# Performance work log

Measured on AMD Instinct MI355X. Metric: run time of the kernel, lower is better.

The kernel has to match this reference:

```python
import jax, jax.numpy as jnp
import numpy as np
from jax import lax

# pywt 'db6' rec_lo (scaling filter). dec_lo = rec_lo[::-1]; pytorch_wavelets
# stores dec filters flipped for conv (=correlation), so analysis correlation
# filters are exactly rec_lo and rec_hi = qmf(rec_lo). Synthesis filters for
# conv_transpose are rec_lo/rec_hi unflipped -> same arrays.
_DB6 = np.array([0.11154074335008017, 0.4946238903983854, 0.7511339080215775,
                 0.3152503517092432, -0.22626469396516913, -0.12976686756709563,
                 0.09750160558707936, 0.02752286553001629, -0.031582039318031156,
                 0.0005538422009938016, 0.004777257511010651, -0.00107730108499558],
                dtype=np.float32)
_QMF = (_DB6[::-1].copy() * ((-1.0) ** np.arange(12))).astype(np.float32)
H0, H1 = jnp.asarray(_DB6), jnp.asarray(_QMF)
LF, J = 12, 3
BATCH, SEQ_LEN, CH = 128, 720, 321
COMP_L = [99, 365, 188, 99]   # [yl, yh1, yh2, yh3] for seq_len=720
OUT_L = [22, 57, 34, 22]      # same decomposition of red_len=104


def afb1d(x):
    """One-level analysis filter bank, mode='symmetric'. x: [B,C,N]."""
    B, C, N = x.shape
    out = (N + LF - 1) // 2                      # pywt dwt_coeff_len (symmetric)
    p = 2 * (out - 1) - N + LF
    xp = jnp.pad(x, ((0, 0), (0, 0), (p // 2, (p + 1) // 2)), mode='symmetric')
    w = jnp.stack([H0, H1])[:, None, :]          # [2,1,LF]
    y = lax.conv_general_dilated(xp.reshape(B * C, 1, -1), w, (2,), 'VALID',
                                 dimension_numbers=('NCH', 'OIH', 'NCH'))
    y = y.reshape(B, C, 2, out)
    return y[:, :, 0], y[:, :, 1]


def sfb1d(lo, hi):
    """One-level synthesis bank == conv_transpose1d(stride=2, padding=LF-2)."""
    B, C, Lin = lo.shape
    z = jnp.stack([lo, hi], axis=2).reshape(B * C, 2, Lin)
    w = jnp.stack([H0[::-1], H1[::-1]])[None]    # [1,2,LF], flipped for corr
    y = lax.conv_general_dilated(z, w, (1,), ((1, 1),), lhs_dilation=(2,),
                                 dimension_numbers=('NCH', 'OIH', 'NCH'))
    return y.reshape(B, C, -1)                   # length 2*Lin + 2 - LF


def sinusoidal_pe(n_pos, d):
    pos = jnp.arange(n_pos, dtype=jnp.float32)[:, None]
    div = jnp.exp(jnp.arange(0, d, 2, dtype=jnp.float32) * (-np.log(10000.0) / d))
    pe = jnp.zeros((n_pos, d), jnp.float32)
    pe = pe.at[:, 0::2].set(jnp.sin(pos * div))
    pe = pe.at[:, 1::2].set(jnp.cos(pos * div[: d // 2]))
    return pe


def _forward(x, qws, qbs, kws, kbs, pws, pbs, iws, als, bes):
    mean = lax.stop_gradient(jnp.mean(x, axis=1, keepdims=True))
    std = lax.stop_gradient(jnp.sqrt(jnp.var(x, axis=1, keepdims=True) + 1e-5))
    xc = jnp.transpose((x - mean) / std, (0, 2, 1))      # [B,C,L]
    yl, yh = xc, []
    for _ in range(J):
        yl, hi = afb1d(yl)
        yh.append(hi)
    decomps = [yl] + yh                                  # lengths COMP_L
    preds = []
    for i, comp in enumerate(decomps):
        B, C, L = comp.shape
        Q = jnp.tanh(comp @ qws[i].T + qbs[i])           # [B,C,L]
        K = jnp.tanh(comp @ kws[i].T + kbs[i])
        scores = jnp.einsum('bcl,bcs->bls', Q, K) / (L ** 0.5)
        weighted = jnp.mean(jnp.tanh(scores), axis=1)    # [B,S] (equal per channel)
        cum = jnp.flip(jnp.cumsum(jnp.flip(weighted, -1), -1), -1)
        P = jax.nn.softmax(cum * als[i][0], axis=-1)
        idxs = jnp.arange(L, dtype=jnp.float32)
        win = jnp.sum(P * idxs, axis=-1)[:, None, None]  # soft truncation [B,1,1]
        mask = jax.nn.sigmoid((idxs[None, None, :] - win) * bes[i][0])
        pred = (comp * mask) @ pws[i].T + pbs[i]         # [B,C,O]
        pred = jax.nn.softmax(iws[i], axis=1) * (pred + sinusoidal_pe(C, pred.shape[-1])[None])
        preds.append(pred)
    ll = preds[0]
    for h in preds[:0:-1]:                               # coarsest high band first
        if ll.shape[-1] > h.shape[-1]:
            ll = ll[..., : h.shape[-1]]
        ll = sfb1d(ll, h)
    return ll, mean, std


def setup_inputs() -> dict:
    key = jax.random.key(0)
    ks = jax.random.split(key, 64)
    inp = {'x': jax.random.normal(ks[0], (BATCH, SEQ_LEN, CH), jnp.float32)}
    k = 1
    for i, (L, O) in enumerate(zip(COMP_L, OUT_L)):
        s = 1.0 / np.sqrt(L)                             # torch Linear default init
        inp[f'qw{i}'] = jax.random.uniform(ks[k], (L, L), jnp.float32, -s, s); k += 1
        inp[f'qb{i}'] = jax.random.uniform(ks[k], (L,), jnp.float32, -s, s); k += 1
        inp[f'kw{i}'] = jax.random.uniform(ks[k], (L, L), jnp.float32, -s, s); k += 1
        inp[f'kb{i}'] = jax.random.uniform(ks[k], (L,), jnp.float32, -s, s); k += 1
        inp[f'pw{i}'] = jnp.full((O, L), 1.0 / L, jnp.float32)
        inp[f'pb{i}'] = jnp.zeros((O,), jnp.float32)
        inp[f'iw{i}'] = jnp.ones((1, CH, O), jnp.float32)
        inp[f'al{i}'] = jnp.full((1,), 10.0, jnp.float32)
        inp[f'be{i}'] = jnp.full((1,), 10.0, jnp.float32)
    return inp


def reference(x, qw0, qb0, kw0, kb0, pw0, pb0, iw0, al0, be0,
              qw1, qb1, kw1, kb1, pw1, pb1, iw1, al1, be1,
              qw2, qb2, kw2, kb2, pw2, pb2, iw2, al2, be2,
              qw3, qb3, kw3, kb3, pw3, pb3, iw3, al3, be3):
    return _forward(x, [qw0, qw1, qw2, qw3], [qb0, qb1, qb2, qb3],
                    [kw0, kw1, kw2, kw3], [kb0, kb1, kb2, kb3],
                    [pw0, pw1, pw2, pw3], [pb0, pb1, pb2, pb3],
                    [iw0, iw1, iw2, iw3], [al0, al1, al2, al3],
                    [be0, be1, be2, be3])
```

## Files before the change

### kernel.cpp

```cpp
#include <hip/hip_runtime.h>
#include <hip/hip_bf16.h>
#include <math.h>

namespace {
constexpr int kB  = 128;
constexpr int kC  = 321;
constexpr int kN0 = 720;
constexpr int kCp = 384;
}

typedef __attribute__((ext_vector_type(8))) short short8;
typedef __attribute__((ext_vector_type(4))) float floatx4;

__constant__ float c_h0[12] = {
  0.11154074335008017f, 0.4946238903983854f, 0.7511339080215775f,
  0.3152503517092432f, -0.22626469396516913f, -0.12976686756709563f,
  0.09750160558707936f, 0.02752286553001629f, -0.031582039318031156f,
  0.0005538422009938016f, 0.004777257511010651f, -0.00107730108499558f};
__constant__ float c_h1[12] = {
  -0.00107730108499558f, -0.004777257511010651f, 0.0005538422009938016f,
  0.031582039318031156f, 0.02752286553001629f, -0.09750160558707936f,
  -0.12976686756709563f, 0.22626469396516913f, 0.3152503517092432f,
  -0.7511339080215775f, 0.4946238903983854f, -0.11154074335008017f};
__constant__ float c_h0r[12] = {
  -0.00107730108499558f, 0.004777257511010651f, 0.0005538422009938016f,
  -0.031582039318031156f, 0.02752286553001629f, 0.09750160558707936f,
  -0.12976686756709563f, -0.22626469396516913f, 0.3152503517092432f,
  0.7511339080215775f, 0.4946238903983854f, 0.11154074335008017f};
__constant__ float c_h1r[12] = {
  -0.11154074335008017f, 0.4946238903983854f, -0.7511339080215775f,
  0.3152503517092432f, 0.22626469396516913f, -0.12976686756709563f,
  -0.09750160558707936f, 0.02752286553001629f, 0.031582039318031156f,
  0.0005538422009938016f, -0.004777257511010651f, -0.00107730108499558f};

__device__ __forceinline__ float fast_tanh(float x) {
  float e = __expf(2.f * x);
  return 1.f - 2.f / (e + 1.f);
}
__device__ __forceinline__ unsigned short f2b(float f) {
  __hip_bfloat16 h = __float2bfloat16(f);
  return __builtin_bit_cast(unsigned short, h);
}

__device__ __forceinline__ void gload16(const unsigned short* g, short* l) {
  __builtin_amdgcn_global_load_lds(
      (const __attribute__((address_space(1))) unsigned int*)g,
      (__attribute__((address_space(3))) unsigned int*)l, 16, 0, 0);
}

__global__ void __launch_bounds__(128) partial_ms_kernel(
    const float* __restrict__ x, float* __restrict__ ps, float* __restrict__ ps2) {
  int b = blockIdx.x, chunk = blockIdx.y;
  int c = blockIdx.z * 128 + threadIdx.x;
  if (c >= kC) return;
  const float* xb = x + (size_t)b * kN0 * kC + c;
  int t0 = chunk * 90;
  float s = 0.f, s2 = 0.f;
#pragma unroll 15
  for (int i = 0; i < 90; ++i) {
    float v = xb[(size_t)(t0 + i) * kC];
    s += v; s2 += v * v;
  }
  ps [(b * 8 + chunk) * kC + c] = s;
  ps2[(b * 8 + chunk) * kC + c] = s2;
}

__global__ void __launch_bounds__(256) finalize_ms_kernel(
    const float* __restrict__ ps, const float* __restrict__ ps2,
    float* __restrict__ mout, float* __restrict__ sout,
    float* __restrict__ meanw, float* __restrict__ invw) {
  int i = blockIdx.x * 256 + threadIdx.x;
  if (i >= kB * kC) return;
  int b = i / kC, c = i - b * kC;
  float s = 0.f, s2 = 0.f;
#pragma unroll
  for (int k = 0; k < 8; ++k) { s += ps[(b * 8 + k) * kC + c]; s2 += ps2[(b * 8 + k) * kC + c]; }
  float mean = s * (1.f / (float)kN0);
  float var = s2 * (1.f / (float)kN0) - mean * mean;
  float sd = sqrtf(var + 1e-5f);
  mout[i] = mean; sout[i] = sd;
  meanw[i] = mean; invw[i] = 1.f / sd;
}

__device__ __forceinline__ int sym_reflect(int t, int N) {
  t = (t < 0) ? (-1 - t) : t;
  t = (t >= N) ? (2 * N - 1 - t) : t;
  return t;
}

template <bool NORM, bool LO_F32, bool LO_BF16>
__global__ void __launch_bounds__(256) dwt_fused_kernel(
    const float* __restrict__ in, const float* __restrict__ meanw,
    const float* __restrict__ invw, float* __restrict__ loF,
    unsigned short* __restrict__ loB, unsigned short* __restrict__ hiB,
    int N, int L, int Lp) {
  __shared__ float xs[138][64];
  __shared__ unsigned short los[64][72];
  __shared__ unsigned short his[64][72];
  const int b = blockIdx.z;
  const int n0 = blockIdx.x * 64, c0 = blockIdx.y * 64;
  const int tid = threadIdx.x;
  const int cl = tid & 63, wv = tid >> 6;
  const int c = c0 + cl;
  const int t0 = 2 * n0 - 10;
  const float* ib = in + (size_t)b * N * kC;
  float mean = 0.f, inv = 1.f;
  if (NORM && c < kC) { mean = meanw[b * kC + c]; inv = invw[b * kC + c]; }
  for (int r = wv; r < 138; r += 4) {
    int t = sym_reflect(t0 + r, N);
    float v = (c < kC) ? ib[(size_t)t * kC + c] : 0.f;
    if (NORM) v = (v - mean) * inv;
    xs[r][cl] = v;
  }
  __syncthreads();
#pragma unroll 4
  for (int k = 0; k < 16; ++k) {
    int nl = wv + 4 * k;
    int n = n0 + nl;
    float a0 = 0.f, a1 = 0.f;
    int base = 2 * nl;
#pragma unroll
    for (int j = 0; j < 12; ++j) {
      float v = xs[base + j][cl];
      a0 += v * c_h0[j]; a1 += v * c_h1[j];
    }
    bool valid = (n < L) && (c < kC);
    if (LO_F32 && valid) loF[((size_t)b * L + n) * kC + c] = a0;
    if (LO_BF16) los[cl][nl] = f2b(valid ? a0 : 0.f);
    his[cl][nl] = f2b(valid ? a1 : 0.f);
  }
  __syncthreads();
  int row = tid >> 2, part = tid & 3;
  size_t dst = ((size_t)b * kCp + c0 + row) * Lp + n0 + part * 16;
  *(uint4*)(hiB + dst)     = *(const uint4*)&his[row][part * 16];
  *(uint4*)(hiB + dst + 8) = *(const uint4*)&his[row][part * 16 + 8];
  if (LO_BF16) {
    *(uint4*)(loB + dst)     = *(const uint4*)&los[row][part * 16];
    *(uint4*)(loB + dst + 8) = *(const uint4*)&los[row][part * 16 + 8];
  }
}

struct WcArgs { const float* src[8]; unsigned short* dst[8]; int L[8]; int Lp[8]; };
__global__ void __launch_bounds__(256) wconv_all_kernel(WcArgs a) {
  int lvl = blockIdx.y;
  int Lp = a.Lp[lvl], L = a.L[lvl];
  int i = blockIdx.x * 256 + threadIdx.x;
  if (i >= Lp * Lp) return;
  int p = i / Lp, l = i - p * Lp;
  a.dst[lvl][i] = f2b((p < L && l < L) ? a.src[lvl][(size_t)p * L + l] : 0.f);
}

struct QKAllArgs {
  const unsigned short* W[8];
  const unsigned short* Xt[4];
  const float* bias[8];
  unsigned short* Y[8];
  int Lp[4], L[4], yOff[4];
};
__global__ void __launch_bounds__(512, 8) qk_all_kernel(QKAllArgs a) {
  const int y = blockIdx.y;
  const int lvl = (y >= a.yOff[1]) + (y >= a.yOff[2]) + (y >= a.yOff[3]);
  const int Lp = a.Lp[lvl], L = a.L[lvl];
  const int pBase = (y - a.yOff[lvl]) * 128;
  const unsigned short* W0 = a.W[2 * lvl]     + (size_t)pBase * Lp;
  const unsigned short* W1 = a.W[2 * lvl + 1] + (size_t)pBase * Lp;
  const int b = blockIdx.z;
  const int cBase = blockIdx.x * 64;
  const int tid = threadIdx.x;
  const int ln = tid & 63, w = tid >> 6;
  __shared__ short smem[2 * 320 * 32];
  floatx4 acc[2][4] = {};
  const unsigned short* Xb = a.Xt[lvl] + ((size_t)b * kCp + cBase) * Lp;
  const int lr = ln >> 2;
  const int ck = (ln & 3) * 8;
  const int nld = (w < 4) ? 3 : 2;
  const int ow0 = (w < 4) ? w * 3 : 12 + (w - 4) * 2;
  const unsigned short* srcs[3];
#pragma unroll
  for (int i = 0; i < 3; ++i) {
    int o = (i < nld) ? (ow0 + i) : ow0;
    int rr = o * 16 + lr;
    const unsigned short* s = (o < 8)  ? (W0 + (size_t)rr * Lp)
                            : (o < 16) ? (W1 + (size_t)(rr - 128) * Lp)
                                       : (Xb + (size_t)(rr - 256) * Lp);
    srcs[i] = s + ck;
  }
  const int nt = Lp >> 5;
#pragma unroll
  for (int i = 0; i < 3; ++i)
    if (i < nld) gload16(srcs[i], &smem[(ow0 + i) * 512]);
  __syncthreads();
  for (int kt = 0; kt < nt; ++kt) {
    if (kt + 1 < nt) {
      const int phn = ((kt + 1) & 1) * 10240;
      const int lc = (kt + 1) << 5;
#pragma unroll
      for (int i = 0; i < 3; ++i)
        if (i < nld) gload16(srcs[i] + lc, &smem[phn + (ow0 + i) * 512]);
    }
    const int ph = (kt & 1) * 10240;
    const int ko = (ln >> 4) * 8;
    const int ar = (w * 16 + (ln & 15)) * 32 + ko;
    short8 aq = *(const short8*)&smem[ph + ar];
    short8 ak = *(const short8*)&smem[ph + 4096 + ar];
    short8 bv[4];
#pragma unroll
    for (int ni = 0; ni < 4; ++ni)
      bv[ni] = *(const short8*)&smem[ph + 8192 + (ni * 16 + (ln & 15)) * 32 + ko];
#pragma unroll
    for (int ni = 0; ni < 4; ++ni) {
      acc[0][ni] = __builtin_amdgcn_mfma_f32_16x16x32_bf16(aq, bv[ni], acc[0][ni], 0, 0, 0);
      acc[1][ni] = __builtin_amdgcn_mfma_f32_16x16x32_bf16(ak, bv[ni], acc[1][ni], 0, 0, 0);
    }
    __syncthreads();
  }
#pragma unroll
  for (int s = 0; s < 2; ++s) {
    const float* bias = a.bias[2 * lvl + s];
    unsigned short* Yd = a.Y[2 * lvl + s];
#pragma unroll
    for (int r = 0; r < 4; ++r) {
      int p = pBase + w * 16 + (ln >> 4) * 4 + r;
      bool pv = (p < L);
      float bvf = pv ? bias[p] : 0.f;
#pragma unroll
      for (int ni = 0; ni < 4; ++ni) {
        int c = cBase + ni * 16 + (ln & 15);
        float v = fast_tanh(acc[s][ni][r] + bvf);
        if (s == 0) { if (!pv) v = 0.f; }
        else        { if (c >= kC) v = 0.f; }
        Yd[((size_t)b * Lp + p) * kCp + c] = f2b(v);
      }
    }
  }
}

struct ScAllArgs {
  const unsigned short* Q[4]; const unsigned short* K[4];
  float* wgt[4];
  int Lp[4], L[4], tOff[4];
  float scale[4];
};
__global__ void __launch_bounds__(512, 8) scores_all_kernel(ScAllArgs a) {
  const int t = blockIdx.x;
  const int lvl = (t >= a.tOff[1]) + (t >= a.tOff[2]) + (t >= a.tOff[3]);
  const int rel = t - a.tOff[lvl];
  const int Lp = a.Lp[lvl], L = a.L[lvl];
  const int pt = Lp >> 7;
  const int sBase = (rel % pt) * 128;
  const int lBase = (rel / pt) * 128;
  const int b = blockIdx.y;
  const int tid = threadIdx.x;
  const int ln = tid & 63, w = tid >> 6;
  const int wm = w & 3, wn = w >> 2;
  __shared__ short smem[2 * 256 * 32];
  __shared__ float red[128];
  floatx4 acc[2][4] = {};
  const unsigned short* Qp = a.Q[lvl] + ((size_t)b * Lp + lBase) * kCp;
  const unsigned short* Kp = a.K[lvl] + ((size_t)b * Lp + sBase) * kCp;
  const int lr = ln >> 2;
  const int ck = (ln & 3) * 8;
  const unsigned short* srcs[2];
#pragma unroll
  for (int i = 0; i < 2; ++i) {
    int o = w * 2 + i;
    int rr = o * 16 + lr;
    srcs[i] = ((o < 8) ? (Qp + (size_t)rr * kCp)
                       : (Kp + (size_t)(rr - 128) * kCp)) + ck;
  }
#pragma unroll
  for (int i = 0; i < 2; ++i) gload16(srcs[i], &smem[(w * 2 + i) * 512]);
  if (tid < 128) red[tid] = 0.f;
  __syncthreads();
  const int nt = kCp >> 5;
  for (int kt = 0; kt < nt; ++kt) {
    if (kt + 1 < nt) {
      const int phn = ((kt + 1) & 1) * 8192;
      const int cc = (kt + 1) << 5;
#pragma unroll
      for (int i = 0; i < 2; ++i) gload16(srcs[i] + cc, &smem[phn + (w * 2 + i) * 512]);
    }
    const int ph = (kt & 1) * 8192;
    const int ko = (ln >> 4) * 8;
    short8 av[2], bv[4];
#pragma unroll
    for (int mi = 0; mi < 2; ++mi)
      av[mi] = *(const short8*)&smem[ph + (wm * 32 + mi * 16 + (ln & 15)) * 32 + ko];
#pragma unroll
    for (int ni = 0; ni < 4; ++ni)
      bv[ni] = *(const short8*)&smem[ph + 4096 + (wn * 64 + ni * 16 + (ln & 15)) * 32 + ko];
#pragma unroll
    for (int mi = 0; mi < 2; ++mi)
#pragma unroll
      for (int ni = 0; ni < 4; ++ni)
        acc[mi][ni] = __builtin_amdgcn_mfma_f32_16x16x32_bf16(av[mi], bv[ni], acc[mi][ni], 0, 0, 0);
    __syncthreads();
  }
  const float scale = a.scale[lvl];
#pragma unroll
  for (int ni = 0; ni < 4; ++ni) {
    float p = 0.f;
#pragma unroll
    for (int mi = 0; mi < 2; ++mi)
#pragma unroll
      for (int r = 0; r < 4; ++r) p += fast_tanh(acc[mi][ni][r] * scale);
    p += __shfl_xor(p, 16);
    p += __shfl_xor(p, 32);
    if ((ln & 48) == 0) atomicAdd(&red[wn * 64 + ni * 16 + (ln & 15)], p);
  }
  __syncthreads();
  if (tid < 128) {
    int s = sBase + tid;
    if (s < L) atomicAdd(&a.wgt[lvl][(size_t)b * L + s], red[tid]);
  }
}

struct WinIwArgs {
  const float* wgt[4]; const float* al[4]; const float* be[4];
  float* mask[4]; int L[4];
  const float* iw[4]; float* sm[4]; int O[4];
};
__global__ void __launch_bounds__(64) winiw_kernel(WinIwArgs a) {
  int bx = blockIdx.x;
  int lane = threadIdx.x;
  if (bx < 512) {
    int lvl = bx >> 7, b = bx & 127;
    int L = a.L[lvl];
    const float* wgt = a.wgt[lvl] + (size_t)b * L;
    float al = a.al[lvl][0], be = a.be[lvl][0];
    float invL = 1.f / (float)L;
    int chunk = (L + 63) >> 6;
    int s0 = lane * chunk;
    float v[6];
    float csum = 0.f;
    for (int i = chunk - 1; i >= 0; --i) {
      int s = s0 + i;
      float xv = (s < L) ? wgt[s] * invL : 0.f;
      csum += xv; v[i] = csum;
    }
    float tot = csum;
    for (int o = 1; o < 64; o <<= 1) {
      float t = __shfl_down(tot, o);
      if (lane + o < 64) tot += t;
    }
    float excl = tot - csum;
    float m = -1e30f;
    for (int i = 0; i < chunk; ++i)
      if (s0 + i < L) m = fmaxf(m, al * (v[i] + excl));
    for (int o = 32; o; o >>= 1) m = fmaxf(m, __shfl_xor(m, o));
    float sum = 0.f, num = 0.f;
    for (int i = 0; i < chunk; ++i) {
      int s = s0 + i;
      if (s < L) { float e = __expf(al * (v[i] + excl) - m); sum += e; num += e * (float)s; }
    }
    for (int o = 32; o; o >>= 1) { sum += __shfl_xor(sum, o); num += __shfl_xor(num, o); }
    float win = num / sum;
    float* mk = a.mask[lvl] + (size_t)b * L;
    for (int i = 0; i < chunk; ++i) {
      int s = s0 + i;
      if (s < L) mk[s] = 1.f / (1.f + __expf(-((float)s - win) * be));
    }
  } else {
    int x = bx - 512;
    int lvl, o;
    if (x < 22) { lvl = 0; o = x; }
    else if (x < 79) { lvl = 1; o = x - 22; }
    else if (x < 113) { lvl = 2; o = x - 79; }
    else { lvl = 3; o = x - 113; }
    int O = a.O[lvl];
    const float* iw = a.iw[lvl];
    float m = -1e30f;
    for (int c = lane; c < kC; c += 64) m = fmaxf(m, iw[c * O + o]);
    for (int k = 32; k; k >>= 1) m = fmaxf(m, __shfl_xor(m, k));
    float sum = 0.f;
    for (int c = lane; c < kC; c += 64) sum += __expf(iw[c * O + o] - m);
    for (int k = 32; k; k >>= 1) sum += __shfl_xor(sum, k);
    float inv = 1.f / sum;
    for (int c = lane; c < kC; c += 64) a.sm[lvl][c * O + o] = __expf(iw[c * O + o] - m) * inv;
  }
}

struct PredAllArgs {
  const unsigned short* Xt[4];
  const float* PW[4]; const float* PB[4]; const float* MK[4]; const float* SM[4];
  float* OUT[4];
  int L[4], Lp[4], O[4];
};
__global__ void __launch_bounds__(256) pred_all_kernel(PredAllArgs a) {
  const int lvl = blockIdx.y;
  const int L = a.L[lvl], Lp = a.Lp[lvl], O = a.O[lvl];
  const float* PW = a.PW[lvl];
  const int b = blockIdx.z;
  const int cBase = blockIdx.x * 128;
  const int tid = threadIdx.x;
  const int ln = tid & 63, w = tid >> 6;
  __shared__ short As[64 * 40];
  __shared__ short Bs[128 * 40];
  floatx4 acc[8] = {};
  const unsigned short* Xb = a.Xt[lvl] + ((size_t)b * kCp + cBase) * Lp;
  const float* mk = a.MK[lvl] + (size_t)b * L;
  for (int lc = 0; lc < Lp; lc += 32) {
    {
      int o = tid >> 2, j0 = (tid & 3) * 8;
      alignas(16) unsigned short tmp[8];
#pragma unroll
      for (int j = 0; j < 8; ++j) {
        int l = lc + j0 + j;
        float v = (o < O && l < L) ? PW[(size_t)o * L + l] * mk[l] : 0.f;
        tmp[j] = f2b(v);
      }
      *(uint4*)&As[o * 40 + j0] = *(const uint4*)tmp;
    }
#pragma unroll
    for (int q = 0; q < 2; ++q) {
      int ch = tid * 2 + q;
      int row = ch >> 2, pos = ch & 3;
      *(uint4*)(&Bs[row * 40 + pos * 8]) = *(const uint4*)(Xb + (size_t)row * Lp + lc + pos * 8);
    }
    __syncthreads();
    short8 av = *(const short8*)&As[(w * 16 + (ln & 15)) * 40 + (ln >> 4) * 8];
#pragma unroll
    for (int ni = 0; ni < 8; ++ni) {
      short8 bb = *(const short8*)&Bs[(ni * 16 + (ln & 15)) * 40 + (ln >> 4) * 8];
      acc[ni] = __builtin_amdgcn_mfma_f32_16x16x32_bf16(av, bb, acc[ni], 0, 0, 0);
    }
    __syncthreads();
  }
  const float negln = -logf(10000.f) / (float)O;
#pragma unroll
  for (int ni = 0; ni < 8; ++ni) {
    int c = cBase + ni * 16 + (ln & 15);
    if (c >= kC) continue;
#pragma unroll
    for (int r = 0; r < 4; ++r) {
      int o = w * 16 + (ln >> 4) * 4 + r;
      if (o >= O) continue;
      float dv = __expf(negln * (float)(2 * (o >> 1)));
      float ang = (float)c * dv;
      float pe = (o & 1) ? cosf(ang) : sinf(ang);
      a.OUT[lvl][((size_t)b * O + o) * kC + c] = a.SM[lvl][c * O + o] * (acc[ni][r] + a.PB[lvl][o] + pe);
    }
  }
}

__global__ void __launch_bounds__(256) sfb_fused_kernel(
    const float* __restrict__ P0, const float* __restrict__ P1,
    const float* __restrict__ P2, const float* __restrict__ P3,
    float* __restrict__ out) {
  __shared__ float p0s[22][32], p3s[22][32], p2s[34][32], p1s[57][32];
  __shared__ float r1s[34][32], r2s[58][32];
  __shared__ float outs[104][33];
  int b = blockIdx.y, c0 = blockIdx.x * 32;
  int tid = threadIdx.x;
  int cl = tid & 31, r = tid >> 5;
  int c = c0 + cl;
  bool cv = c < kC;
  for (int o = r; o < 22; o += 8) {
    p0s[o][cl] = cv ? P0[((size_t)b * 22 + o) * kC + c] : 0.f;
    p3s[o][cl] = cv ? P3[((size_t)b * 22 + o) * kC + c] : 0.f;
  }
  for (int o = r; o < 34; o += 8) p2s[o][cl] = cv ? P2[((size_t)b * 34 + o) * kC + c] : 0.f;
  for (int o = r; o < 57; o += 8) p1s[o][cl] = cv ? P1[((size_t)b * 57 + o) * kC + c] : 0.f;
  __syncthreads();
  for (int n = r; n < 34; n += 8) {
    float acc = 0.f;
#pragma unroll
    for (int j = 0; j < 12; ++j) {
      int m = n + j - 1;
      if (m < 0 || (m & 1)) continue;
      int i = m >> 1;
      if (i >= 22) continue;
      acc += c_h0r[j] * p0s[i][cl] + c_h1r[j] * p3s[i][cl];
    }
    r1s[n][cl] = acc;
  }
  __syncthreads();
  for (int n = r; n < 58; n += 8) {
    float acc = 0.f;
#pragma unroll
    for (int j = 0; j < 12; ++j) {
      int m = n + j - 1;
      if (m < 0 || (m & 1)) continue;
      int i = m >> 1;
      if (i >= 34) continue;
      acc += c_h0r[j] * r1s[i][cl] + c_h1r[j] * p2s[i][cl];
    }
    r2s[n][cl] = acc;
  }
  __syncthreads();
  for (int n = r; n < 104; n += 8) {
    float acc = 0.f;
#pragma unroll
    for (int j = 0; j < 12; ++j) {
      int m = n + j - 1;
      if (m < 0 || (m & 1)) continue;
      int i = m >> 1;
      if (i >= 57) continue;
      acc += c_h0r[j] * r2s[i][cl] + c_h1r[j] * p1s[i][cl];
    }
    outs[n][cl] = acc;
  }
  __syncthreads();
  for (int idx = tid; idx < 32 * 104; idx += 256) {
    int ci = idx / 104, n = idx - ci * 104;
    int cg = c0 + ci;
    if (cg < kC) out[((size_t)b * kC + cg) * 104 + n] = outs[n][ci];
  }
}

extern "C" void kernel_launch(void* const* d_in, const int* in_sizes, int n_in,
                              void* d_out, int out_size, void* d_ws, size_t ws_size,
                              hipStream_t stream) {
  (void)in_sizes; (void)n_in; (void)out_size; (void)ws_size;
  const float* x = (const float*)d_in[0];
  auto inp = [&](int lvl, int j) { return (const float*)d_in[1 + 9 * lvl + j]; };

  float* outf = (float*)d_out;
  float* mout = outf + (size_t)kB * kC * 104;
  float* sout = mout + (size_t)kB * kC;

  float* Wp = (float*)d_ws;
  size_t off = 0;
  auto alloc = [&](size_t n) { float* p = Wp + off; off += (n + 63) & ~(size_t)63; return p; };

  float* LO1 = alloc((size_t)kB * 365 * kC);
  float* LO2 = alloc((size_t)kB * 188 * kC);
  unsigned short* Xt1 = (unsigned short*)alloc((size_t)kB * kCp * 384 / 2);
  unsigned short* Xt2 = (unsigned short*)alloc((size_t)kB * kCp * 256 / 2);
  unsigned short* Xt0 = (unsigned short*)alloc((size_t)kB * kCp * 128 / 2);
  unsigned short* Xt3 = (unsigned short*)alloc((size_t)kB * kCp * 128 / 2);
  unsigned short* KbfAll = (unsigned short*)alloc((size_t)kB * kCp * 896 / 2);
  unsigned short* Wpv[8];
  for (int i = 0; i < 8; ++i)
    Wpv[i] = (unsigned short*)alloc((size_t)384 * 384 / 2);
  float* wgtAll = alloc((size_t)kB * (99 + 365 + 188 + 99));
  float* M0 = alloc((size_t)kB * 99);  float* M1 = alloc((size_t)kB * 365);
  float* M2 = alloc((size_t)kB * 188); float* M3 = alloc((size_t)kB * 99);
  float* S0 = alloc((size_t)kC * 22);  float* S1 = alloc((size_t)kC * 57);
  float* S2 = alloc((size_t)kC * 34);  float* S3 = alloc((size_t)kC * 22);
  float* P0 = alloc((size_t)kB * 22 * kC); float* P1 = alloc((size_t)kB * 57 * kC);
  float* P2 = alloc((size_t)kB * 34 * kC); float* P3 = alloc((size_t)kB * 22 * kC);
  float* ps   = alloc((size_t)kB * 8 * kC);
  float* ps2  = alloc((size_t)kB * 8 * kC);
  float* meanw = alloc((size_t)kB * kC);
  float* invw  = alloc((size_t)kB * kC);
  unsigned short* QbfAll = (unsigned short*)LO1;

  const int Lc[4]  = {99, 365, 188, 99};
  const int Lpv[4] = {128, 384, 256, 128};
  const int Ov[4]  = {22, 57, 34, 22};
  const int prefLp[4] = {0, 128, 512, 768};
  const int wOff[4] = {0, 99, 99 + 365, 99 + 365 + 188};
  unsigned short* Qlvl[4]; unsigned short* Klvl[4];
  for (int i = 0; i < 4; ++i) {
    Qlvl[i] = QbfAll + (size_t)kB * kCp * prefLp[i];
    Klvl[i] = KbfAll + (size_t)kB * kCp * prefLp[i];
  }
  const unsigned short* Xts[4] = {Xt0, Xt1, Xt2, Xt3};
  float* masks[4] = {M0, M1, M2, M3};
  float* smws[4]  = {S0, S1, S2, S3};
  float* preds[4] = {P0, P1, P2, P3};

  partial_ms_kernel<<<dim3(kB, 8, 3), 128, 0, stream>>>(x, ps, ps2);
  finalize_ms_kernel<<<(kB * kC + 255) / 256, 256, 0, stream>>>(ps, ps2, mout, sout, meanw, invw);

  dwt_fused_kernel<true, true, false><<<dim3(6, kCp / 64, kB), 256, 0, stream>>>(
      x, meanw, invw, LO1, nullptr, Xt1, kN0, 365, 384);
  dwt_fused_kernel<false, true, false><<<dim3(4, kCp / 64, kB), 256, 0, stream>>>(
      LO1, nullptr, nullptr, LO2, nullptr, Xt2, 365, 188, 256);
  dwt_fused_kernel<false, false, true><<<dim3(2, kCp / 64, kB), 256, 0, stream>>>(
      LO2, nullptr, nullptr, nullptr, Xt0, Xt3, 188, 99, 128);

  {
    WcArgs wa;
    for (int i = 0; i < 4; ++i) {
      wa.src[2 * i] = inp(i, 0); wa.src[2 * i + 1] = inp(i, 2);
      wa.dst[2 * i] = Wpv[2 * i]; wa.dst[2 * i + 1] = Wpv[2 * i + 1];
      wa.L[2 * i] = wa.L[2 * i + 1] = Lc[i];
      wa.Lp[2 * i] = wa.Lp[2 * i + 1] = Lpv[i];
    }
    wconv_all_kernel<<<dim3(576, 8), 256, 0, stream>>>(wa);
  }
  hipMemsetAsync(wgtAll, 0, (size_t)kB * (99 + 365 + 188 + 99) * sizeof(float), stream);

  {
    QKAllArgs qa;
    for (int i = 0; i < 4; ++i) {
      qa.W[2 * i] = Wpv[2 * i]; qa.W[2 * i + 1] = Wpv[2 * i + 1];
      qa.bias[2 * i] = inp(i, 1); qa.bias[2 * i + 1] = inp(i, 3);
      qa.Y[2 * i] = Qlvl[i]; qa.Y[2 * i + 1] = Klvl[i];
      qa.Xt[i] = Xts[i]; qa.Lp[i] = Lpv[i]; qa.L[i] = Lc[i];
    }
    qa.yOff[0] = 0; qa.yOff[1] = 1; qa.yOff[2] = 4; qa.yOff[3] = 6;
    qk_all_kernel<<<dim3(kCp / 64, 7, kB), 512, 0, stream>>>(qa);
  }

  {
    ScAllArgs sa;
    for (int i = 0; i < 4; ++i) {
      sa.Q[i] = Qlvl[i]; sa.K[i] = Klvl[i];
      sa.wgt[i] = wgtAll + (size_t)kB * wOff[i];
      sa.Lp[i] = Lpv[i]; sa.L[i] = Lc[i];
      sa.scale[i] = 1.0f / sqrtf((float)Lc[i]);
    }
    sa.tOff[0] = 0; sa.tOff[1] = 1; sa.tOff[2] = 10; sa.tOff[3] = 14;
    scores_all_kernel<<<dim3(15, kB), 512, 0, stream>>>(sa);
  }

  {
    WinIwArgs wa;
    for (int i = 0; i < 4; ++i) {
      wa.wgt[i] = wgtAll + (size_t)kB * wOff[i];
      wa.al[i] = inp(i, 7); wa.be[i] = inp(i, 8);
      wa.mask[i] = masks[i]; wa.L[i] = Lc[i];
      wa.iw[i] = inp(i, 6); wa.sm[i] = smws[i]; wa.O[i] = Ov[i];
    }
    winiw_kernel<<<512 + 135, 64, 0, stream>>>(wa);
  }

  {
    PredAllArgs pa;
    for (int i = 0; i < 4; ++i) {
      pa.Xt[i] = Xts[i]; pa.PW[i] = inp(i, 4); pa.PB[i] = inp(i, 5);
      pa.MK[i] = masks[i]; pa.SM[i] = smws[i]; pa.OUT[i] = preds[i];
      pa.L[i] = Lc[i]; pa.Lp[i] = Lpv[i]; pa.O[i] = Ov[i];
    }
    pred_all_kernel<<<dim3(kCp / 128, 4, kB), 256, 0, stream>>>(pa);
  }

  sfb_fused_kernel<<<dim3(11, kB), 256, 0, stream>>>(P0, P1, P2, P3, outf);
}
```

Before: 795.0 us.

## Swizzle LDS tiles in QK/scores GEMMs, stage QK output, remap score blocks

Applies an XOR/rotation swizzle to the global-to-LDS load offsets and the matching MFMA fragment reads in both the QK projection and scores kernels, to remove LDS bank conflicts. The QK epilogue now writes the tanh output into swizzled shared memory and then stores 16-byte vectors to global memory, replacing scattered 2-byte stores. The scores kernel switches to a 1D grid with a block-index remap that spreads consecutive blocks across XCD-style groups for better cache locality. These add extra index arithmetic and a barrier, and the swizzle must stay consistent between the load and read sides.

Result: faster. 763.8 us (-3.9%).

```diff
diff --git a/kernel.cpp b/kernel.cpp
--- a/kernel.cpp
+++ b/kernel.cpp
@@ -172,7 +172,7 @@
   floatx4 acc[2][4] = {};
   const unsigned short* Xb = a.Xt[lvl] + ((size_t)b * kCp + cBase) * Lp;
   const int lr = ln >> 2;
-  const int ck = (ln & 3) * 8;
+  const int kOfs = ((((ln & 3) - ((ln >> 3) & 3)) & 3)) * 8;
   const int nld = (w < 4) ? 3 : 2;
   const int ow0 = (w < 4) ? w * 3 : 12 + (w - 4) * 2;
   const unsigned short* srcs[3];
@@ -183,8 +183,9 @@
     const unsigned short* s = (o < 8)  ? (W0 + (size_t)rr * Lp)
                             : (o < 16) ? (W1 + (size_t)(rr - 128) * Lp)
                                        : (Xb + (size_t)(rr - 256) * Lp);
-    srcs[i] = s + ck;
-  }
+    srcs[i] = s + kOfs;
+  }
+  const int sc = ((((ln >> 4) + ((ln >> 1) & 3)) & 3)) * 8;
   const int nt = Lp >> 5;
 #pragma unroll
   for (int i = 0; i < 3; ++i)
@@ -193,20 +194,18 @@
   for (int kt = 0; kt < nt; ++kt) {
     if (kt + 1 < nt) {
       const int phn = ((kt + 1) & 1) * 10240;
-      const int lc = (kt + 1) << 5;
 #pragma unroll
       for (int i = 0; i < 3; ++i)
-        if (i < nld) gload16(srcs[i] + lc, &smem[phn + (ow0 + i) * 512]);
+        if (i < nld) { srcs[i] += 32; gload16(srcs[i], &smem[phn + (ow0 + i) * 512]); }
     }
     const int ph = (kt & 1) * 10240;
-    const int ko = (ln >> 4) * 8;
-    const int ar = (w * 16 + (ln & 15)) * 32 + ko;
+    const int ar = (w * 16 + (ln & 15)) * 32 + sc;
     short8 aq = *(const short8*)&smem[ph + ar];
     short8 ak = *(const short8*)&smem[ph + 4096 + ar];
     short8 bv[4];
 #pragma unroll
     for (int ni = 0; ni < 4; ++ni)
-      bv[ni] = *(const short8*)&smem[ph + 8192 + (ni * 16 + (ln & 15)) * 32 + ko];
+      bv[ni] = *(const short8*)&smem[ph + 8192 + (ni * 16 + (ln & 15)) * 32 + sc];
 #pragma unroll
     for (int ni = 0; ni < 4; ++ni) {
       acc[0][ni] = __builtin_amdgcn_mfma_f32_16x16x32_bf16(aq, bv[ni], acc[0][ni], 0, 0, 0);
@@ -214,23 +213,41 @@
     }
     __syncthreads();
   }
+  short* yq = smem;
+  short* yk = smem + 8192;
 #pragma unroll
   for (int s = 0; s < 2; ++s) {
     const float* bias = a.bias[2 * lvl + s];
-    unsigned short* Yd = a.Y[2 * lvl + s];
+    short* dstL = s ? yk : yq;
 #pragma unroll
     for (int r = 0; r < 4; ++r) {
-      int p = pBase + w * 16 + (ln >> 4) * 4 + r;
+      int pl = w * 16 + (ln >> 4) * 4 + r;
+      int p = pBase + pl;
       bool pv = (p < L);
       float bvf = pv ? bias[p] : 0.f;
 #pragma unroll
       for (int ni = 0; ni < 4; ++ni) {
-        int c = cBase + ni * 16 + (ln & 15);
+        int cl = ni * 16 + (ln & 15);
         float v = fast_tanh(acc[s][ni][r] + bvf);
         if (s == 0) { if (!pv) v = 0.f; }
-        else        { if (c >= kC) v = 0.f; }
-        Yd[((size_t)b * Lp + p) * kCp + c] = f2b(v);
+        else        { if (cBase + cl >= kC) v = 0.f; }
+        dstL[pl * 64 + (cl ^ ((pl & 7) << 3))] = (short)f2b(v);
       }
+    }
+  }
+  __syncthreads();
+#pragma unroll
+  for (int s = 0; s < 2; ++s) {
+    unsigned short* Yd = a.Y[2 * lvl + s];
+    const short* srcL = s ? yk : yq;
+#pragma unroll
+    for (int j = 0; j < 2; ++j) {
+      int idx = tid * 2 + j;
+      int row = idx >> 3;
+      int ch = idx & 7;
+      int pch = ch ^ (row & 7);
+      uint4 vv = *(const uint4*)&srcL[row * 64 + pch * 8];
+      *(uint4*)(Yd + ((size_t)b * Lp + pBase + row) * kCp + cBase + ch * 8) = vv;
     }
   }
 }
@@ -242,14 +259,16 @@
   float scale[4];
 };
 __global__ void __launch_bounds__(512, 8) scores_all_kernel(ScAllArgs a) {
-  const int t = blockIdx.x;
+  const int bid = blockIdx.x;
+  const int wg = (bid & 7) * 240 + (bid >> 3);
+  const int t = wg % 15;
+  const int b = wg / 15;
   const int lvl = (t >= a.tOff[1]) + (t >= a.tOff[2]) + (t >= a.tOff[3]);
   const int rel = t - a.tOff[lvl];
   const int Lp = a.Lp[lvl], L = a.L[lvl];
   const int pt = Lp >> 7;
   const int sBase = (rel % pt) * 128;
   const int lBase = (rel / pt) * 128;
-  const int b = blockIdx.y;
   const int tid = threadIdx.x;
   const int ln = tid & 63, w = tid >> 6;
   const int wm = w & 3, wn = w >> 2;
@@ -259,15 +278,16 @@
   const unsigned short* Qp = a.Q[lvl] + ((size_t)b * Lp + lBase) * kCp;
   const unsigned short* Kp = a.K[lvl] + ((size_t)b * Lp + sBase) * kCp;
   const int lr = ln >> 2;
-  const int ck = (ln & 3) * 8;
+  const int kOfs = ((((ln & 3) - ((ln >> 3) & 3)) & 3)) * 8;
   const unsigned short* srcs[2];
 #pragma unroll
   for (int i = 0; i < 2; ++i) {
     int o = w * 2 + i;
     int rr = o * 16 + lr;
     srcs[i] = ((o < 8) ? (Qp + (size_t)rr * kCp)
-                       : (Kp + (size_t)(rr - 128) * kCp)) + ck;
-  }
+                       : (Kp + (size_t)(rr - 128) * kCp)) + kOfs;
+  }
+  const int sc = ((((ln >> 4) + ((ln >> 1) & 3)) & 3)) * 8;
 #pragma unroll
   for (int i = 0; i < 2; ++i) gload16(srcs[i], &smem[(w * 2 + i) * 512]);
   if (tid < 128) red[tid] = 0.f;
@@ -276,19 +296,17 @@
   for (int kt = 0; kt < nt; ++kt) {
     if (kt + 1 < nt) {
       const int phn = ((kt + 1) & 1) * 8192;
-      const int cc = (kt + 1) << 5;
-#pragma unroll
-      for (int i = 0; i < 2; ++i) gload16(srcs[i] + cc, &smem[phn + (w * 2 + i) * 512]);
+#pragma unroll
+      for (int i = 0; i < 2; ++i) { srcs[i] += 32; gload16(srcs[i], &smem[phn + (w * 2 + i) * 512]); }
     }
     const int ph = (kt & 1) * 8192;
-    const int ko = (ln >> 4) * 8;
     short8 av[2], bv[4];
 #pragma unroll
     for (int mi = 0; mi < 2; ++mi)
-      av[mi] = *(const short8*)&smem[ph + (wm * 32 + mi * 16 + (ln & 15)) * 32 + ko];
+      av[mi] = *(const short8*)&smem[ph + (wm * 32 + mi * 16 + (ln & 15)) * 32 + sc];
 #pragma unroll
     for (int ni = 0; ni < 4; ++ni)
-      bv[ni] = *(const short8*)&smem[ph + 4096 + (wn * 64 + ni * 16 + (ln & 15)) * 32 + ko];
+      bv[ni] = *(const short8*)&smem[ph + 4096 + (wn * 64 + ni * 16 + (ln & 15)) * 32 + sc];
 #pragma unroll
     for (int mi = 0; mi < 2; ++mi)
 #pragma unroll
@@ -604,7 +622,7 @@
       sa.scale[i] = 1.0f / sqrtf((float)Lc[i]);
     }
     sa.tOff[0] = 0; sa.tOff[1] = 1; sa.tOff[2] = 10; sa.tOff[3] = 14;
-    scores_all_kernel<<<dim3(15, kB), 512, 0, stream>>>(sa);
+    scores_all_kernel<<<15 * kB, 512, 0, stream>>>(sa);
   }
 
   {
```

## Rework QK and score GEMMs with 32x32 MFMA, triple buffering, swizzled LDS

Applied to the files above, without the earlier changes.

Both GEMM kernels now use 32x32x16 bf16 MFMA instead of 16x16x32 and a three-stage LDS ring with explicit vmcnt waits and raw barriers in place of double buffering. Shared-memory reads use XOR-swizzled columns to avoid bank conflicts. The QK kernel doubles its channel tile to 128 and writes output through LDS with 16-byte coalesced stores. The scores kernel drops to 256 threads on a flattened grid that is remapped to interleave blocks. The goal is more math per LDS load, better load/compute overlap and fewer global store transactions, at the cost of more registers and LDS per block and lower occupancy.

Measured after the change: 781.3 us. About the same (-1.7%).

```diff
diff --git a/kernel.cpp b/kernel.cpp
--- a/kernel.cpp
+++ b/kernel.cpp
@@ -11,6 +11,11 @@
 
 typedef __attribute__((ext_vector_type(8))) short short8;
 typedef __attribute__((ext_vector_type(4))) float floatx4;
+typedef __attribute__((ext_vector_type(16))) float floatx16;
+
+__device__ __forceinline__ floatx16 mfma32(short8 a, short8 b, floatx16 c) {
+  return __builtin_amdgcn_mfma_f32_32x32x16_bf16(a, b, c, 0, 0, 0);
+}
 
 __constant__ float c_h0[12] = {
   0.11154074335008017f, 0.4946238903983854f, 0.7511339080215775f,
@@ -157,7 +162,7 @@
   unsigned short* Y[8];
   int Lp[4], L[4], yOff[4];
 };
-__global__ void __launch_bounds__(512, 8) qk_all_kernel(QKAllArgs a) {
+__global__ void __launch_bounds__(512, 4) qk_all_kernel(QKAllArgs a) {
   const int y = blockIdx.y;
   const int lvl = (y >= a.yOff[1]) + (y >= a.yOff[2]) + (y >= a.yOff[3]);
   const int Lp = a.Lp[lvl], L = a.L[lvl];
@@ -165,72 +170,119 @@
   const unsigned short* W0 = a.W[2 * lvl]     + (size_t)pBase * Lp;
   const unsigned short* W1 = a.W[2 * lvl + 1] + (size_t)pBase * Lp;
   const int b = blockIdx.z;
-  const int cBase = blockIdx.x * 64;
+  const int cBase = blockIdx.x * 128;
   const int tid = threadIdx.x;
   const int ln = tid & 63, w = tid >> 6;
-  __shared__ short smem[2 * 320 * 32];
-  floatx4 acc[2][4] = {};
+  const int wm = w & 3, wn = w >> 2;
+  __shared__ __align__(16) short smem[3 * 384 * 32];
+  floatx16 accQ[2] = {}, accK[2] = {};
   const unsigned short* Xb = a.Xt[lvl] + ((size_t)b * kCp + cBase) * Lp;
   const int lr = ln >> 2;
-  const int ck = (ln & 3) * 8;
-  const int nld = (w < 4) ? 3 : 2;
-  const int ow0 = (w < 4) ? w * 3 : 12 + (w - 4) * 2;
+  const int srcC = ((ln & 3) ^ (lr & 3)) * 8;
   const unsigned short* srcs[3];
 #pragma unroll
   for (int i = 0; i < 3; ++i) {
-    int o = (i < nld) ? (ow0 + i) : ow0;
+    int o = w * 3 + i;
     int rr = o * 16 + lr;
     const unsigned short* s = (o < 8)  ? (W0 + (size_t)rr * Lp)
                             : (o < 16) ? (W1 + (size_t)(rr - 128) * Lp)
                                        : (Xb + (size_t)(rr - 256) * Lp);
-    srcs[i] = s + ck;
-  }
+    srcs[i] = s + srcC;
+  }
+  auto stage = [&](int buf, int lc) {
+#pragma unroll
+    for (int i = 0; i < 3; ++i)
+      gload16(srcs[i] + lc, &smem[buf * 12288 + (w * 3 + i) * 512]);
+  };
+  const int rl = ln & 31, sel = ln >> 5, sw = ln & 3;
+  const int kc0 = ((sel) ^ sw) * 8;
+  const int kc1 = ((2 + sel) ^ sw) * 8;
+  const int aOff  = (wm * 32 + rl) * 32;
+  const int akOff = 4096 + aOff;
+  const int bOff0 = 8192 + (wn * 64 + rl) * 32;
+  const int bOff1 = bOff0 + 1024;
   const int nt = Lp >> 5;
-#pragma unroll
-  for (int i = 0; i < 3; ++i)
-    if (i < nld) gload16(srcs[i], &smem[(ow0 + i) * 512]);
-  __syncthreads();
+  stage(0, 0);
+  stage(1, 32);
+  int bufn = 2, lc = 64, bc = 0;
   for (int kt = 0; kt < nt; ++kt) {
-    if (kt + 1 < nt) {
-      const int phn = ((kt + 1) & 1) * 10240;
-      const int lc = (kt + 1) << 5;
-#pragma unroll
-      for (int i = 0; i < 3; ++i)
-        if (i < nld) gload16(srcs[i] + lc, &smem[phn + (ow0 + i) * 512]);
-    }
-    const int ph = (kt & 1) * 10240;
-    const int ko = (ln >> 4) * 8;
-    const int ar = (w * 16 + (ln & 15)) * 32 + ko;
-    short8 aq = *(const short8*)&smem[ph + ar];
-    short8 ak = *(const short8*)&smem[ph + 4096 + ar];
-    short8 bv[4];
-#pragma unroll
-    for (int ni = 0; ni < 4; ++ni)
-      bv[ni] = *(const short8*)&smem[ph + 8192 + (ni * 16 + (ln & 15)) * 32 + ko];
-#pragma unroll
-    for (int ni = 0; ni < 4; ++ni) {
-      acc[0][ni] = __builtin_amdgcn_mfma_f32_16x16x32_bf16(aq, bv[ni], acc[0][ni], 0, 0, 0);
-      acc[1][ni] = __builtin_amdgcn_mfma_f32_16x16x32_bf16(ak, bv[ni], acc[1][ni], 0, 0, 0);
-    }
-    __syncthreads();
-  }
-#pragma unroll
-  for (int s = 0; s < 2; ++s) {
-    const float* bias = a.bias[2 * lvl + s];
-    unsigned short* Yd = a.Y[2 * lvl + s];
-#pragma unroll
-    for (int r = 0; r < 4; ++r) {
-      int p = pBase + w * 16 + (ln >> 4) * 4 + r;
-      bool pv = (p < L);
-      float bvf = pv ? bias[p] : 0.f;
-#pragma unroll
-      for (int ni = 0; ni < 4; ++ni) {
-        int c = cBase + ni * 16 + (ln & 15);
-        float v = fast_tanh(acc[s][ni][r] + bvf);
-        if (s == 0) { if (!pv) v = 0.f; }
-        else        { if (c >= kC) v = 0.f; }
-        Yd[((size_t)b * Lp + p) * kCp + c] = f2b(v);
-      }
+    if (kt + 1 < nt) asm volatile("s_waitcnt vmcnt(3)" ::: "memory");
+    else             asm volatile("s_waitcnt vmcnt(0)" ::: "memory");
+    __builtin_amdgcn_s_barrier();
+    __builtin_amdgcn_sched_barrier(0);
+    if (kt + 2 < nt) {
+      stage(bufn, lc);
+      lc += 32;
+      bufn = (bufn == 2) ? 0 : bufn + 1;
+    }
+    const int ph = bc * 12288;
+    short8 a0 = *(const short8*)&smem[ph + aOff + kc0];
+    short8 k0 = *(const short8*)&smem[ph + akOff + kc0];
+    short8 b0 = *(const short8*)&smem[ph + bOff0 + kc0];
+    short8 b1 = *(const short8*)&smem[ph + bOff1 + kc0];
+    accQ[0] = mfma32(a0, b0, accQ[0]); accQ[1] = mfma32(a0, b1, accQ[1]);
+    accK[0] = mfma32(k0, b0, accK[0]); accK[1] = mfma32(k0, b1, accK[1]);
+    a0 = *(const short8*)&smem[ph + aOff + kc1];
+    k0 = *(const short8*)&smem[ph + akOff + kc1];
+    b0 = *(const short8*)&smem[ph + bOff0 + kc1];
+    b1 = *(const short8*)&smem[ph + bOff1 + kc1];
+    accQ[0] = mfma32(a0, b0, accQ[0]); accQ[1] = mfma32(a0, b1, accQ[1]);
+    accK[0] = mfma32(k0, b0, accK[0]); accK[1] = mfma32(k0, b1, accK[1]);
+    bc = (bc == 2) ? 0 : bc + 1;
+  }
+  __syncthreads();
+  short* bnc = smem;
+  const int cl = wn * 64 + rl;
+  const bool c0v = (cBase + cl) < kC, c1v = (cBase + cl + 32) < kC;
+  {
+    const float* bias = a.bias[2 * lvl];
+#pragma unroll
+    for (int reg = 0; reg < 16; ++reg) {
+      int pl = wm * 32 + (reg & 3) + 8 * (reg >> 2) + 4 * sel;
+      int p = pBase + pl;
+      bool pv = p < L;
+      float bq = pv ? bias[p] : 0.f;
+      float v0 = fast_tanh(accQ[0][reg] + bq); if (!pv) v0 = 0.f;
+      float v1 = fast_tanh(accQ[1][reg] + bq); if (!pv) v1 = 0.f;
+      bnc[pl * 136 + cl]      = (short)f2b(v0);
+      bnc[pl * 136 + cl + 32] = (short)f2b(v1);
+    }
+  }
+  __syncthreads();
+  {
+    unsigned short* Yd = a.Y[2 * lvl];
+#pragma unroll
+    for (int j = 0; j < 4; ++j) {
+      int idx = tid + j * 512;
+      int row = idx >> 4, ch = idx & 15;
+      *(uint4*)(Yd + ((size_t)b * Lp + pBase + row) * kCp + cBase + ch * 8) =
+          *(const uint4*)&bnc[row * 136 + ch * 8];
+    }
+  }
+  __syncthreads();
+  {
+    const float* bias = a.bias[2 * lvl + 1];
+#pragma unroll
+    for (int reg = 0; reg < 16; ++reg) {
+      int pl = wm * 32 + (reg & 3) + 8 * (reg >> 2) + 4 * sel;
+      int p = pBase + pl;
+      bool pv = p < L;
+      float bq = pv ? bias[p] : 0.f;
+      float v0 = fast_tanh(accK[0][reg] + bq); if (!c0v) v0 = 0.f;
+      float v1 = fast_tanh(accK[1][reg] + bq); if (!c1v) v1 = 0.f;
+      bnc[pl * 136 + cl]      = (short)f2b(v0);
+      bnc[pl * 136 + cl + 32] = (short)f2b(v1);
+    }
+  }
+  __syncthreads();
+  {
+    unsigned short* Yd = a.Y[2 * lvl + 1];
+#pragma unroll
+    for (int j = 0; j < 4; ++j) {
+      int idx = tid + j * 512;
+      int row = idx >> 4, ch = idx & 15;
+      *(uint4*)(Yd + ((size_t)b * Lp + pBase + row) * kCp + cBase + ch * 8) =
+          *(const uint4*)&bnc[row * 136 + ch * 8];
     }
   }
 }
@@ -241,72 +293,86 @@
   int Lp[4], L[4], tOff[4];
   float scale[4];
 };
-__global__ void __launch_bounds__(512, 8) scores_all_kernel(ScAllArgs a) {
-  const int t = blockIdx.x;
+__global__ void __launch_bounds__(256, 4) scores_all_kernel(ScAllArgs a) {
+  const int bid = blockIdx.x;
+  const int wg = (bid & 7) * 240 + (bid >> 3);
+  const int t = wg % 15;
+  const int b = wg / 15;
   const int lvl = (t >= a.tOff[1]) + (t >= a.tOff[2]) + (t >= a.tOff[3]);
   const int rel = t - a.tOff[lvl];
   const int Lp = a.Lp[lvl], L = a.L[lvl];
   const int pt = Lp >> 7;
   const int sBase = (rel % pt) * 128;
   const int lBase = (rel / pt) * 128;
-  const int b = blockIdx.y;
   const int tid = threadIdx.x;
   const int ln = tid & 63, w = tid >> 6;
-  const int wm = w & 3, wn = w >> 2;
-  __shared__ short smem[2 * 256 * 32];
+  const int wm = w & 1, wn = w >> 1;
+  __shared__ __align__(16) short smem[3 * 256 * 32];
   __shared__ float red[128];
-  floatx4 acc[2][4] = {};
+  floatx16 acc[2][2] = {};
   const unsigned short* Qp = a.Q[lvl] + ((size_t)b * Lp + lBase) * kCp;
   const unsigned short* Kp = a.K[lvl] + ((size_t)b * Lp + sBase) * kCp;
   const int lr = ln >> 2;
-  const int ck = (ln & 3) * 8;
-  const unsigned short* srcs[2];
-#pragma unroll
-  for (int i = 0; i < 2; ++i) {
-    int o = w * 2 + i;
+  const int srcC = ((ln & 3) ^ (lr & 3)) * 8;
+  const unsigned short* srcs[4];
+#pragma unroll
+  for (int i = 0; i < 4; ++i) {
+    int o = w * 4 + i;
     int rr = o * 16 + lr;
     srcs[i] = ((o < 8) ? (Qp + (size_t)rr * kCp)
-                       : (Kp + (size_t)(rr - 128) * kCp)) + ck;
-  }
-#pragma unroll
-  for (int i = 0; i < 2; ++i) gload16(srcs[i], &smem[(w * 2 + i) * 512]);
+                       : (Kp + (size_t)(rr - 128) * kCp)) + srcC;
+  }
+  auto stage = [&](int buf, int cc) {
+#pragma unroll
+    for (int i = 0; i < 4; ++i)
+      gload16(srcs[i] + cc, &smem[buf * 8192 + (w * 4 + i) * 512]);
+  };
+  const int rl = ln & 31, sel = ln >> 5, sw = ln & 3;
+  const int kc0 = ((sel) ^ sw) * 8;
+  const int kc1 = ((2 + sel) ^ sw) * 8;
+  const int aOff0 = (wm * 64 + rl) * 32, aOff1 = aOff0 + 1024;
+  const int bOff0 = 4096 + (wn * 64 + rl) * 32, bOff1 = bOff0 + 1024;
   if (tid < 128) red[tid] = 0.f;
-  __syncthreads();
   const int nt = kCp >> 5;
+  stage(0, 0);
+  stage(1, 32);
+  int bufn = 2, cc = 64, bc = 0;
   for (int kt = 0; kt < nt; ++kt) {
-    if (kt + 1 < nt) {
-      const int phn = ((kt + 1) & 1) * 8192;
-      const int cc = (kt + 1) << 5;
-#pragma unroll
-      for (int i = 0; i < 2; ++i) gload16(srcs[i] + cc, &smem[phn + (w * 2 + i) * 512]);
-    }
-    const int ph = (kt & 1) * 8192;
-    const int ko = (ln >> 4) * 8;
-    short8 av[2], bv[4];
-#pragma unroll
-    for (int mi = 0; mi < 2; ++mi)
-      av[mi] = *(const short8*)&smem[ph + (wm * 32 + mi * 16 + (ln & 15)) * 32 + ko];
-#pragma unroll
-    for (int ni = 0; ni < 4; ++ni)
-      bv[ni] = *(const short8*)&smem[ph + 4096 + (wn * 64 + ni * 16 + (ln & 15)) * 32 + ko];
-#pragma unroll
-    for (int mi = 0; mi < 2; ++mi)
-#pragma unroll
-      for (int ni = 0; ni < 4; ++ni)
-        acc[mi][ni] = __builtin_amdgcn_mfma_f32_16x16x32_bf16(av[mi], bv[ni], acc[mi][ni], 0, 0, 0);
-    __syncthreads();
+    if (kt + 1 < nt) asm volatile("s_waitcnt vmcnt(4)" ::: "memory");
+    else             asm volatile("s_waitcnt vmcnt(0)" ::: "memory");
+    __builtin_amdgcn_s_barrier();
+    __builtin_amdgcn_sched_barrier(0);
+    if (kt + 2 < nt) {
+      stage(bufn, cc);
+      cc += 32;
+      bufn = (bufn == 2) ? 0 : bufn + 1;
+    }
+    const int ph = bc * 8192;
+    short8 a0 = *(const short8*)&smem[ph + aOff0 + kc0];
+    short8 a1 = *(const short8*)&smem[ph + aOff1 + kc0];
+    short8 b0 = *(const short8*)&smem[ph + bOff0 + kc0];
+    short8 b1 = *(const short8*)&smem[ph + bOff1 + kc0];
+    acc[0][0] = mfma32(a0, b0, acc[0][0]); acc[0][1] = mfma32(a0, b1, acc[0][1]);
+    acc[1][0] = mfma32(a1, b0, acc[1][0]); acc[1][1] = mfma32(a1, b1, acc[1][1]);
+    a0 = *(const short8*)&smem[ph + aOff0 + kc1];
+    a1 = *(const short8*)&smem[ph + aOff1 + kc1];
+    b0 = *(const short8*)&smem[ph + bOff0 + kc1];
+    b1 = *(const short8*)&smem[ph + bOff1 + kc1];
+    acc[0][0] = mfma32(a0, b0, acc[0][0]); acc[0][1] = mfma32(a0, b1, acc[0][1]);
+    acc[1][0] = mfma32(a1, b0, acc[1][0]); acc[1][1] = mfma32(a1, b1, acc[1][1]);
+    bc = (bc == 2) ? 0 : bc + 1;
   }
   const float scale = a.scale[lvl];
 #pragma unroll
-  for (int ni = 0; ni < 4; ++ni) {
+  for (int sf = 0; sf < 2; ++sf) {
     float p = 0.f;
 #pragma unroll
-    for (int mi = 0; mi < 2; ++mi)
-#pragma unroll
-      for (int r = 0; r < 4; ++r) p += fast_tanh(acc[mi][ni][r] * scale);
-    p += __shfl_xor(p, 16);
+    for (int lf = 0; lf < 2; ++lf)
+#pragma unroll
+      for (int reg = 0; reg < 16; ++reg)
+        p += fast_tanh(acc[lf][sf][reg] * scale);
     p += __shfl_xor(p, 32);
-    if ((ln & 48) == 0) atomicAdd(&red[wn * 64 + ni * 16 + (ln & 15)], p);
+    if (ln < 32) atomicAdd(&red[wn * 64 + sf * 32 + ln], p);
   }
   __syncthreads();
   if (tid < 128) {
@@ -592,7 +658,7 @@
       qa.Xt[i] = Xts[i]; qa.Lp[i] = Lpv[i]; qa.L[i] = Lc[i];
     }
     qa.yOff[0] = 0; qa.yOff[1] = 1; qa.yOff[2] = 4; qa.yOff[3] = 6;
-    qk_all_kernel<<<dim3(kCp / 64, 7, kB), 512, 0, stream>>>(qa);
+    qk_all_kernel<<<dim3(kCp / 128, 7, kB), 512, 0, stream>>>(qa);
   }
 
   {
@@ -604,7 +670,7 @@
       sa.scale[i] = 1.0f / sqrtf((float)Lc[i]);
     }
     sa.tOff[0] = 0; sa.tOff[1] = 1; sa.tOff[2] = 10; sa.tOff[3] = 14;
-    scores_all_kernel<<<dim3(15, kB), 512, 0, stream>>>(sa);
+    scores_all_kernel<<<15 * kB, 256, 0, stream>>>(sa);
   }
 
   {
```
